# Performance work log

Hardware: AMD Instinct MI355X
Metric: run time of the kernel (lower is better)

Reference implementation:

```python
import jax, jax.numpy as jnp
import numpy as np

B, D, N = 1024, 2048, 16384
TEMP, LAMBDA2, MU = 0.05, 0.5, 1.0
EPS = 1e-12


def l2norm(x):
    # F.normalize(x, dim=1): x / max(||x||, eps)
    n = jnp.sqrt(jnp.sum(x * x, axis=1, keepdims=True))
    return x / jnp.maximum(n, EPS)


def cdist(x, f):
    # Euclidean distance matrix [B, N]
    x2 = jnp.sum(x * x, axis=1, keepdims=True)          # [B,1]
    f2 = jnp.sum(f * f, axis=1)                          # [N]
    sq = x2 + f2[None, :] - 2.0 * (x @ f.T)
    return jnp.sqrt(jnp.maximum(sq, 0.0))


def cross_entropy(logits, targets):
    logp = jax.nn.log_softmax(logits, axis=1)
    return -jnp.mean(logp[jnp.arange(logits.shape[0]), targets])


def setup_inputs() -> dict:
    key = jax.random.key(0)
    ks = jax.random.split(key, 10)
    inp = {
        'inputs': jax.random.normal(ks[0], (B, D), jnp.float32),
        'inputs_up': jax.random.normal(ks[1], (B, D), jnp.float32),
        'inputs_down': jax.random.normal(ks[2], (B, D), jnp.float32),
        'inputs_teacher': jax.random.normal(ks[3], (B, D), jnp.float32),
        'inputs_up_teacher': jax.random.normal(ks[4], (B, D), jnp.float32),
        'inputs_down_teacher': jax.random.normal(ks[5], (B, D), jnp.float32),
        'targets': jax.random.randint(ks[6], (B,), 0, N, jnp.int32),
        'epoch': 1,
        # memory bank buffers (unit-normalized rows, as maintained by CM updates)
        'features': l2norm(jax.random.normal(ks[7], (N, D), jnp.float32)),
        'features_up': l2norm(jax.random.normal(ks[8], (N, D), jnp.float32)),
        'features_down': l2norm(jax.random.normal(ks[9], (N, D), jnp.float32)),
    }
    return inp


def reference(inputs, inputs_up, inputs_down, inputs_teacher, inputs_up_teacher,
              inputs_down_teacher, targets, epoch, features, features_up, features_down):
    x = l2norm(inputs)
    xu = l2norm(inputs_up)
    xd = l2norm(inputs_down)
    t = l2norm(inputs_teacher)
    tu = l2norm(inputs_up_teacher)
    td = l2norm(inputs_down_teacher)

    # softmax over Euclidean distances to memory (used as 'logits' for CE below)
    x_soft = jax.nn.softmax(cdist(x, features), axis=1)
    xu_soft = jax.nn.softmax(cdist(xu, features_up), axis=1)
    xd_soft = jax.nn.softmax(cdist(xd, features_down), axis=1)

    # CM forward: similarity logits against memory, scaled by temperature
    out = (x @ features.T) / TEMP
    out_u = (xu @ features_up.T) / TEMP
    out_d = (xd @ features_down.T) / TEMP

    # MSELoss(reduce=False)(a,b).mean(0).sum()
    ld = jnp.sum(jnp.mean((x - t) ** 2, axis=0))
    ld_u = jnp.sum(jnp.mean((xu - tu) ** 2, axis=0))
    ld_d = jnp.sum(jnp.mean((xd - td) ** 2, axis=0))

    loss = ((1.0 - LAMBDA2) * (cross_entropy(out, targets) + MU * ld + cross_entropy(x_soft, targets))
            + LAMBDA2 * (cross_entropy(out_u, targets) + MU * ld_u + cross_entropy(xu_soft, targets))
            + LAMBDA2 * (cross_entropy(out_d, targets) + MU * ld_d + cross_entropy(xd_soft, targets)))
    return loss
```

## Files before the change

### kernel.cpp

```cpp
#include <hip/hip_runtime.h>

constexpr int BB = 1024;
constexpr int DD = 2048;
constexpr int NN = 16384;
constexpr float TEMP   = 0.05f;
constexpr float LAMBDA2 = 0.5f;
constexpr float MU      = 1.0f;
constexpr float EPSN    = 1e-12f;

typedef __bf16  bf16x8  __attribute__((ext_vector_type(8)));
typedef unsigned short ushort8 __attribute__((ext_vector_type(8)));
typedef float   floatx4 __attribute__((ext_vector_type(4)));

__device__ inline unsigned short f32_to_bf16(float f) {
  unsigned int u = __builtin_bit_cast(unsigned int, f);
  u += 0x7fffu + ((u >> 16) & 1u);
  return (unsigned short)(u >> 16);
}

__device__ inline float block_sum256(float v, float* sbuf) {
#pragma unroll
  for (int o = 32; o > 0; o >>= 1) v += __shfl_down(v, o, 64);
  int lane = threadIdx.x & 63, w = threadIdx.x >> 6;
  __syncthreads();
  if (lane == 0) sbuf[w] = v;
  __syncthreads();
  return sbuf[0] + sbuf[1] + sbuf[2] + sbuf[3];
}

__device__ inline float block_max256(float v, float* sbuf) {
#pragma unroll
  for (int o = 32; o > 0; o >>= 1) v = fmaxf(v, __shfl_down(v, o, 64));
  int lane = threadIdx.x & 63, w = threadIdx.x >> 6;
  __syncthreads();
  if (lane == 0) sbuf[w] = v;
  __syncthreads();
  return fmaxf(fmaxf(sbuf[0], sbuf[1]), fmaxf(sbuf[2], sbuf[3]));
}

__global__ void __launch_bounds__(256) norm_mse_kernel(
    const float* __restrict__ X, const float* __restrict__ T,
    unsigned short* __restrict__ Xb, float* __restrict__ mse_part) {
  __shared__ float sbuf[4];
  const int b = blockIdx.x;
  const float4* xr = (const float4*)(X + (size_t)b * DD);
  const float4* tr = (const float4*)(T + (size_t)b * DD);
  float4 xv[2], tv[2];
  float sx = 0.f, st = 0.f;
#pragma unroll
  for (int i = 0; i < 2; ++i) {
    int idx = i * 256 + threadIdx.x;
    xv[i] = xr[idx];  tv[i] = tr[idx];
    sx += xv[i].x*xv[i].x + xv[i].y*xv[i].y + xv[i].z*xv[i].z + xv[i].w*xv[i].w;
    st += tv[i].x*tv[i].x + tv[i].y*tv[i].y + tv[i].z*tv[i].z + tv[i].w*tv[i].w;
  }
  sx = block_sum256(sx, sbuf);
  st = block_sum256(st, sbuf);
  const float rx = 1.f / fmaxf(sqrtf(sx), EPSN);
  const float rt = 1.f / fmaxf(sqrtf(st), EPSN);
  float ms = 0.f;
  ushort4* xb4 = (ushort4*)(Xb + (size_t)b * DD);
#pragma unroll
  for (int i = 0; i < 2; ++i) {
    int idx = i * 256 + threadIdx.x;
    float xn, tn, d;
    ushort4 o;
    xn = xv[i].x * rx; tn = tv[i].x * rt; d = xn - tn; ms += d * d; o.x = f32_to_bf16(xn);
    xn = xv[i].y * rx; tn = tv[i].y * rt; d = xn - tn; ms += d * d; o.y = f32_to_bf16(xn);
    xn = xv[i].z * rx; tn = tv[i].z * rt; d = xn - tn; ms += d * d; o.z = f32_to_bf16(xn);
    xn = xv[i].w * rx; tn = tv[i].w * rt; d = xn - tn; ms += d * d; o.w = f32_to_bf16(xn);
    xb4[idx] = o;
  }
  ms = block_sum256(ms, sbuf);
  if (threadIdx.x == 0) mse_part[b] = ms;
}

__global__ void __launch_bounds__(256) feat_convert_kernel(
    const float* __restrict__ F, unsigned short* __restrict__ Fb) {
  const int stride = gridDim.x * 256;
  const float4* fr = (const float4*)F;
  constexpr int TOT = NN * DD / 8;
  for (int i = blockIdx.x * 256 + threadIdx.x; i < TOT; i += stride) {
    float4 a = fr[i * 2], b = fr[i * 2 + 1];
    ushort8 o;
    o[0] = f32_to_bf16(a.x); o[1] = f32_to_bf16(a.y);
    o[2] = f32_to_bf16(a.z); o[3] = f32_to_bf16(a.w);
    o[4] = f32_to_bf16(b.x); o[5] = f32_to_bf16(b.y);
    o[6] = f32_to_bf16(b.z); o[7] = f32_to_bf16(b.w);
    *(ushort8*)(Fb + (size_t)i * 8) = o;
  }
}

constexpr int BM = 256, BN = 256, BK = 64;
constexpr int KT = DD / BK;

__device__ inline void async_copy16(const void* g, void* l) {
  __builtin_amdgcn_global_load_lds(
      (const __attribute__((address_space(1))) unsigned int*)g,
      (__attribute__((address_space(3))) unsigned int*)l, 16, 0, 0);
}

__device__ __forceinline__ void stage_half(const unsigned short* src,
                                           unsigned short* dstRegion, int tid8) {
  async_copy16(src, dstRegion + tid8);
  async_copy16(src + 64 * DD, dstRegion + 4096 + tid8);
}

__global__ void __launch_bounds__(512, 2) gemm_bt_kernel(
    const unsigned short* __restrict__ A,
    const unsigned short* __restrict__ Bm,
    float* __restrict__ C) {
  __shared__ __align__(16) unsigned short As[2 * 2 * 128 * 64];
  __shared__ __align__(16) unsigned short Bs[2 * 2 * 128 * 64];

  const int tid  = threadIdx.x;
  const int lane = tid & 63;
  const int wave = tid >> 6;
  const int l16  = lane & 15;
  const int quad = lane >> 4;
  const int rm   = wave >> 2;
  const int rn   = wave & 3;
  const int m0 = blockIdx.y * BM;
  const int n0 = blockIdx.x * BN;

  const int xr = l16 & 7;
  const int cs[2] = { (quad ^ xr) * 8, ((4 + quad) ^ xr) * 8 };

  const int srow = tid >> 3;
  const int lcol = ((tid & 7) ^ (srow & 7)) * 8;
  const int tid8 = tid * 8;
  const unsigned short* aSrcT = A  + (size_t)(m0 + srow) * DD + lcol;
  const unsigned short* bSrcT = Bm + (size_t)(n0 + srow) * DD + lcol;

  floatx4 acc[8][4] = {};

  stage_half(aSrcT,                As,          tid8);
  stage_half(aSrcT + 128 * DD,     As + 8192,   tid8);
  stage_half(bSrcT,                Bs,          tid8);
  stage_half(bSrcT + 128 * DD,     Bs + 8192,   tid8);
  stage_half(bSrcT + BK,           Bs + 16384,  tid8);
  stage_half(bSrcT + 128 * DD + BK, Bs + 24576, tid8);
  asm volatile("s_waitcnt vmcnt(4)" ::: "memory");
  asm volatile("s_barrier" ::: "memory");

  for (int t = 0; t < KT; ++t) {
    const int c = t & 1, o = c ^ 1;
    const unsigned short* aB = As + c * 16384 + rm * 8192 + l16 * 64;
    const unsigned short* bB = Bs + c * 16384 + (rn >> 1) * 8192
                                  + (rn & 1) * 4096 + l16 * 64;
    const int kA = (t + 1 < KT) ? (t + 1) * BK : 0;
    const int kB = (t + 2 < KT) ? (t + 2) * BK : 0;
    const unsigned short* aS = aSrcT + kA;
    const unsigned short* bS = bSrcT + kB;

    const unsigned short* stSrc[4] = { aS, aS + 128 * DD, bS, bS + 128 * DD };
    unsigned short* stDst[4] = { As + o * 16384, As + o * 16384 + 8192,
                                 Bs + c * 16384, Bs + c * 16384 + 8192 };

    bf16x8 bf[4][2];
#pragma unroll
    for (int mp = 0; mp < 4; ++mp) {
      if (mp == 0) {
#pragma unroll
        for (int n = 0; n < 4; ++n)
#pragma unroll
          for (int s = 0; s < 2; ++s)
            bf[n][s] = __builtin_bit_cast(bf16x8,
                         *(const ushort8*)(bB + n * 1024 + cs[s]));
      }
      bf16x8 af[2][2];
#pragma unroll
      for (int mi = 0; mi < 2; ++mi)
#pragma unroll
        for (int s = 0; s < 2; ++s)
          af[mi][s] = __builtin_bit_cast(bf16x8,
                        *(const ushort8*)(aB + (mp * 2 + mi) * 1024 + cs[s]));

      stage_half(stSrc[mp], stDst[mp], tid8);

      asm volatile("s_barrier" ::: "memory");
      __builtin_amdgcn_s_setprio(1);
#pragma unroll
      for (int mi = 0; mi < 2; ++mi)
#pragma unroll
        for (int n = 0; n < 4; ++n)
#pragma unroll
          for (int s = 0; s < 2; ++s)
            acc[mp * 2 + mi][n] = __builtin_amdgcn_mfma_f32_16x16x32_bf16(
                af[mi][s], bf[n][s], acc[mp * 2 + mi][n], 0, 0, 0);
      __builtin_amdgcn_s_setprio(0);
      if (mp == 3)
        asm volatile("s_waitcnt vmcnt(4)" ::: "memory");
      asm volatile("s_barrier" ::: "memory");
    }
  }

#pragma unroll
  for (int r = 0; r < 8; ++r) {
    const int grow = m0 + rm * 128 + r * 16 + quad * 4;
#pragma unroll
    for (int n = 0; n < 4; ++n) {
      const int gcol = n0 + rn * 64 + n * 16 + l16;
#pragma unroll
      for (int i = 0; i < 4; ++i)
        C[(size_t)(grow + i) * NN + gcol] = acc[r][n][i];
    }
  }
}

__global__ void __launch_bounds__(256) rowstat_kernel(
    const float* __restrict__ sim, const int* __restrict__ tgt,
    float* __restrict__ ce_part) {
  __shared__ float sbuf[4];
  const int b = blockIdx.x;
  const float4* sr = (const float4*)(sim + (size_t)b * NN);
  constexpr float INV_T = 1.0f / TEMP;

  float4 dv[16];
  float m1 = -1e30f, s1 = 0.f;
  float m2 = -1e30f;
#pragma unroll
  for (int i = 0; i < 16; ++i) {
    const int idx = i * 256 + threadIdx.x;
    float4 s = sr[idx];
    float lm = fmaxf(fmaxf(s.x, s.y), fmaxf(s.z, s.w)) * INV_T;
    if (lm > m1) { s1 *= expf(m1 - lm); m1 = lm; }
    s1 += expf(s.x * INV_T - m1) + expf(s.y * INV_T - m1)
        + expf(s.z * INV_T - m1) + expf(s.w * INV_T - m1);
    float4 d;
    d.x = sqrtf(fmaxf(2.f - 2.f * s.x, 0.f));
    d.y = sqrtf(fmaxf(2.f - 2.f * s.y, 0.f));
    d.z = sqrtf(fmaxf(2.f - 2.f * s.z, 0.f));
    d.w = sqrtf(fmaxf(2.f - 2.f * s.w, 0.f));
    dv[i] = d;
    m2 = fmaxf(m2, fmaxf(fmaxf(d.x, d.y), fmaxf(d.z, d.w)));
  }
  const float M1 = block_max256(m1, sbuf);
  const float s1t = block_sum256(s1 * expf(m1 - M1), sbuf);
  const float M2 = block_max256(m2, sbuf);

  float s2 = 0.f;
#pragma unroll
  for (int i = 0; i < 16; ++i) {
    float4 d = dv[i];
    s2 += expf(d.x - M2) + expf(d.y - M2) + expf(d.z - M2) + expf(d.w - M2);
  }
  const float s2t = block_sum256(s2, sbuf);
  const float invs2 = 1.f / s2t;

  float sp = 0.f;
#pragma unroll
  for (int i = 0; i < 16; ++i) {
    float4 d = dv[i];
    sp += expf(expf(d.x - M2) * invs2) + expf(expf(d.y - M2) * invs2)
        + expf(expf(d.z - M2) * invs2) + expf(expf(d.w - M2) * invs2);
  }
  const float spt = block_sum256(sp, sbuf);

  if (threadIdx.x == 0) {
    const int t = tgt[b];
    const float st = sim[(size_t)b * NN + t];
    const float dt = sqrtf(fmaxf(2.f - 2.f * st, 0.f));
    const float pt = expf(dt - M2) * invs2;
    const float ce1 = M1 + logf(s1t) - st * INV_T;
    const float ce2 = logf(spt) - pt;
    ce_part[b] = ce1 + ce2;
  }
}

__global__ void __launch_bounds__(256) final_reduce_kernel(
    const float* __restrict__ mse_part,
    const float* __restrict__ ce_part,
    float* __restrict__ loss) {
  __shared__ float sbuf[4];
  float s = 0.f;
  for (int i = threadIdx.x; i < 3 * BB; i += 256) {
    const float w = (i < BB) ? (1.0f - LAMBDA2) : LAMBDA2;
    s += w * (MU * mse_part[i] + ce_part[i]);
  }
  s = block_sum256(s, sbuf);
  if (threadIdx.x == 0) loss[0] = s * (1.0f / (float)BB);
}

extern "C" void kernel_launch(void* const* d_in, const int* in_sizes, int n_in,
                              void* d_out, int out_size, void* d_ws, size_t ws_size,
                              hipStream_t stream) {
  const float* xin[3] = {(const float*)d_in[0], (const float*)d_in[1], (const float*)d_in[2]};
  const float* tin[3] = {(const float*)d_in[3], (const float*)d_in[4], (const float*)d_in[5]};
  const int*   targets = (const int*)d_in[6];
  const float* fin[3] = {(const float*)d_in[8], (const float*)d_in[9], (const float*)d_in[10]};

  char* ws = (char*)d_ws;
  size_t off = 0;
  unsigned short* featb = (unsigned short*)(ws + off); off += (size_t)NN * DD * 2;
  float*          sim   = (float*)(ws + off);          off += (size_t)BB * NN * 4;
  unsigned short* xb    = (unsigned short*)(ws + off); off += (size_t)BB * DD * 2;
  float*          msep  = (float*)(ws + off);          off += (size_t)3 * BB * 4;
  float*          cep   = (float*)(ws + off);          off += (size_t)3 * BB * 4;

  for (int i = 0; i < 3; ++i) {
    norm_mse_kernel<<<BB, 256, 0, stream>>>(xin[i], tin[i], xb, msep + i * BB);
    feat_convert_kernel<<<4096, 256, 0, stream>>>(fin[i], featb);
    gemm_bt_kernel<<<dim3(NN / BN, BB / BM), 512, 0, stream>>>(xb, featb, sim);
    rowstat_kernel<<<BB, 256, 0, stream>>>(sim, targets, cep + i * BB);
  }
  final_reduce_kernel<<<1, 256, 0, stream>>>(msep, cep, (float*)d_out);
}
```

Measured before the change: 752.9 us.

## Replace interleaved 8-wave GEMM pipeline with simple double-buffered stage-then-compute loop

Replaces the fine-grained schedule, which interleaved quarter-tile global-to-LDS stages with MFMA groups and kept B two tiles ahead, with a plain double buffer. Each half-iteration issues all four stage loads for the next K tile, then does all LDS reads and MFMAs for the current tile in two K-substeps, then waits for all loads and barriers once. This cuts the barriers per K tile from eight to one and simplifies the prefetch-distance bookkeeping. In exchange there is less overlap between loads and compute, since the full load must finish before each barrier, and register pressure rises from holding eight A fragments at once.

```diff
diff --git a/kernel.cpp b/kernel.cpp
--- a/kernel.cpp
+++ b/kernel.cpp
@@ -134,63 +134,47 @@
 
   floatx4 acc[8][4] = {};
 
-  stage_half(aSrcT,                As,          tid8);
-  stage_half(aSrcT + 128 * DD,     As + 8192,   tid8);
-  stage_half(bSrcT,                Bs,          tid8);
-  stage_half(bSrcT + 128 * DD,     Bs + 8192,   tid8);
-  stage_half(bSrcT + BK,           Bs + 16384,  tid8);
-  stage_half(bSrcT + 128 * DD + BK, Bs + 24576, tid8);
-  asm volatile("s_waitcnt vmcnt(4)" ::: "memory");
+  stage_half(aSrcT,            As,        tid8);
+  stage_half(aSrcT + 128 * DD, As + 8192, tid8);
+  stage_half(bSrcT,            Bs,        tid8);
+  stage_half(bSrcT + 128 * DD, Bs + 8192, tid8);
+  asm volatile("s_waitcnt vmcnt(0)" ::: "memory");
   asm volatile("s_barrier" ::: "memory");
 
-  for (int t = 0; t < KT; ++t) {
-    const int c = t & 1, o = c ^ 1;
-    const unsigned short* aB = As + c * 16384 + rm * 8192 + l16 * 64;
-    const unsigned short* bB = Bs + c * 16384 + (rn >> 1) * 8192
-                                  + (rn & 1) * 4096 + l16 * 64;
-    const int kA = (t + 1 < KT) ? (t + 1) * BK : 0;
-    const int kB = (t + 2 < KT) ? (t + 2) * BK : 0;
-    const unsigned short* aS = aSrcT + kA;
-    const unsigned short* bS = bSrcT + kB;
-
-    const unsigned short* stSrc[4] = { aS, aS + 128 * DD, bS, bS + 128 * DD };
-    unsigned short* stDst[4] = { As + o * 16384, As + o * 16384 + 8192,
-                                 Bs + c * 16384, Bs + c * 16384 + 8192 };
-
-    bf16x8 bf[4][2];
-#pragma unroll
-    for (int mp = 0; mp < 4; ++mp) {
-      if (mp == 0) {
+  for (int i = 0; i < KT / 2; ++i) {
+#pragma unroll
+    for (int h = 0; h < 2; ++h) {
+      const int ob = h ^ 1;
+      const int kst = (h == 0) ? (2 * i + 1) : ((2 * i + 2) & (KT - 1));
+      const unsigned short* aS = aSrcT + kst * BK;
+      const unsigned short* bS = bSrcT + kst * BK;
+      stage_half(aS,            As + ob * 16384,        tid8);
+      stage_half(aS + 128 * DD, As + ob * 16384 + 8192, tid8);
+      stage_half(bS,            Bs + ob * 16384,        tid8);
+      stage_half(bS + 128 * DD, Bs + ob * 16384 + 8192, tid8);
+
+      const unsigned short* aB = As + h * 16384 + rm * 8192 + l16 * 64;
+      const unsigned short* bB = Bs + h * 16384 + (rn >> 1) * 8192
+                                    + (rn & 1) * 4096 + l16 * 64;
+#pragma unroll
+      for (int s = 0; s < 2; ++s) {
+        bf16x8 bf[4], af[8];
 #pragma unroll
         for (int n = 0; n < 4; ++n)
-#pragma unroll
-          for (int s = 0; s < 2; ++s)
-            bf[n][s] = __builtin_bit_cast(bf16x8,
-                         *(const ushort8*)(bB + n * 1024 + cs[s]));
+          bf[n] = __builtin_bit_cast(bf16x8, *(const ushort8*)(bB + n * 1024 + cs[s]));
+#pragma unroll
+        for (int r = 0; r < 8; ++r)
+          af[r] = __builtin_bit_cast(bf16x8, *(const ushort8*)(aB + r * 1024 + cs[s]));
+        __builtin_amdgcn_s_setprio(1);
+#pragma unroll
+        for (int r = 0; r < 8; ++r)
+#pragma unroll
+          for (int n = 0; n < 4; ++n)
+            acc[r][n] = __builtin_amdgcn_mfma_f32_16x16x32_bf16(
+                af[r], bf[n], acc[r][n], 0, 0, 0);
+        __builtin_amdgcn_s_setprio(0);
       }
-      bf16x8 af[2][2];
-#pragma unroll
-      for (int mi = 0; mi < 2; ++mi)
-#pragma unroll
-        for (int s = 0; s < 2; ++s)
-          af[mi][s] = __builtin_bit_cast(bf16x8,
-                        *(const ushort8*)(aB + (mp * 2 + mi) * 1024 + cs[s]));
-
-      stage_half(stSrc[mp], stDst[mp], tid8);
-
-      asm volatile("s_barrier" ::: "memory");
-      __builtin_amdgcn_s_setprio(1);
-#pragma unroll
-      for (int mi = 0; mi < 2; ++mi)
-#pragma unroll
-        for (int n = 0; n < 4; ++n)
-#pragma unroll
-          for (int s = 0; s < 2; ++s)
-            acc[mp * 2 + mi][n] = __builtin_amdgcn_mfma_f32_16x16x32_bf16(
-                af[mi][s], bf[n][s], acc[mp * 2 + mi][n], 0, 0, 0);
-      __builtin_amdgcn_s_setprio(0);
-      if (mp == 3)
-        asm volatile("s_waitcnt vmcnt(4)" ::: "memory");
+      asm volatile("s_waitcnt vmcnt(0)" ::: "memory");
       asm volatile("s_barrier" ::: "memory");
     }
   }
```

Result: faster. 710.2 us (-5.7%).
